# Kernel optimization log

Measured on AMD Instinct MI355X. Metric: run time of the kernel, lower is better.

The kernel has to match this reference:

```python
import jax, jax.numpy as jnp
import numpy as np

B, S, EMBED, DK, DV, M = 8, 1024, 1024, 512, 512, 64


def setup_inputs() -> dict:
    key = jax.random.key(0)
    ks = jax.random.split(key, 9)
    query_in = jax.random.normal(ks[0], (B, S, EMBED), dtype=jnp.float32)
    key_in = jax.random.normal(ks[1], (B, S, EMBED), dtype=jnp.float32)
    value_in = jax.random.normal(ks[2], (B, S, EMBED), dtype=jnp.float32)
    lim = 1.0 / np.sqrt(EMBED)  # nn.Linear default init range
    u = lambda k, shape: jax.random.uniform(k, shape, minval=-lim, maxval=lim, dtype=jnp.float32)
    return {
        'query_in': query_in, 'key_in': key_in, 'value_in': value_in,
        'Wq': u(ks[3], (DK, EMBED)), 'bq': u(ks[4], (DK,)),
        'Wk': u(ks[5], (DK, EMBED)), 'bk': u(ks[6], (DK,)),
        'Wv': u(ks[7], (DV, EMBED)), 'bv': u(ks[8], (DV,)),
    }


def _select_landmarks(k_proj, m):
    # Original code runs recursive RLS sampling (random, host-side) over the m
    # segment-rows of key.reshape(B, m, seg, d) and gathers m of them back,
    # then flattens to (B, S, d). We use a deterministic data-dependent
    # selection (rows ranked by squared norm) with identical gather structure.
    Bb, Ss, d = k_proj.shape
    seg = Ss // m
    kr = k_proj.reshape(Bb, m, seg, d)
    scores = jnp.sum(kr * kr, axis=(2, 3))                      # [B, m]
    idx = jnp.argsort(-scores, axis=1)                          # [B, m]
    land = jnp.take_along_axis(kr, idx[:, :, None, None], axis=1)
    return land.reshape(Bb, Ss, d)                              # [B, S, d]


def reference(query_in, key_in, value_in, Wq, bq, Wk, bk, Wv, bv):
    scaling = DK ** -0.25  # 1/sqrt(sqrt(d_k)), applied to both q and k
    q = (jnp.einsum('bse,de->bsd', query_in, Wq) + bq) * scaling
    k = (jnp.einsum('bse,de->bsd', key_in, Wk) + bk) * scaling
    v = jnp.einsum('bse,de->bsd', value_in, Wv) + bv

    kl = _select_landmarks(k, M)                                # [B, S, DK]
    # is_decoder_self_attn is hard-coded True upstream -> q_landmarks = q,
    # so kernel_2 == kernel_1.
    kernel_1 = jax.nn.softmax(jnp.einsum('bqd,bkd->bqk', q, kl), axis=-1)
    kernel_2 = kernel_1
    kernel_3 = jax.nn.softmax(jnp.einsum('bqd,bkd->bqk', q, k), axis=-1)

    k2_inv = jnp.linalg.pinv(kernel_2)                          # [B, S, S] batched SVD
    out = jnp.einsum('bqk,bkd->bqd', jnp.einsum('bqm,bmk->bqk', kernel_1, k2_inv),
                     jnp.einsum('bqk,bkd->bqd', kernel_3, v))
    # dropout is identity in eval mode
    return out
```

## Files before the change

### kernel.cpp

```cpp
#include <hip/hip_runtime.h>
#include <hip/hip_bf16.h>

#define SS   1024
#define DKK  512

typedef __hip_bfloat16 bf16;
typedef __attribute__((ext_vector_type(8))) short s16x8;
typedef __attribute__((ext_vector_type(8))) unsigned short u16x8;
typedef __attribute__((ext_vector_type(4))) float f32x4;

#define WS_W(z)  ((48ull << 20) + ((size_t)(z) << 20))
#define WS_ST    (51ull << 20)
#define WS_Q     (52ull << 20)
#define WS_K     (60ull << 20)
#define WS_VT    (68ull << 20)
#define WS_LG    (0ull)

__device__ __forceinline__ void async_ld16(const void* g, void* s) {
  __builtin_amdgcn_global_load_lds(
      (const __attribute__((address_space(1))) void*)g,
      (__attribute__((address_space(3))) void*)s, 16, 0, 0);
}

__device__ __forceinline__ unsigned short f2bfu(float f) {
  return __builtin_bit_cast(unsigned short, __float2bfloat16(f));
}
__device__ __forceinline__ float bfu2f(unsigned short u) {
  unsigned int i = ((unsigned int)u) << 16;
  return __builtin_bit_cast(float, i);
}

__global__ __launch_bounds__(256)
void convert_w(const float* __restrict__ w0, const float* __restrict__ w1,
               const float* __restrict__ w2, char* __restrict__ ws)
{
  const int bx = blockIdx.x;
  const int z = bx >> 8, local = bx & 255;
  const float* src = (z == 0) ? w0 : (z == 1) ? w1 : w2;
  unsigned short* dst = (unsigned short*)(ws + WS_W(z));
  const int i = local * 2048 + threadIdx.x * 8;
  const float4* s = (const float4*)(src + i);
  float4 a = s[0], b = s[1];
  ushort4 o0, o1;
  o0.x = f2bfu(a.x); o0.y = f2bfu(a.y); o0.z = f2bfu(a.z); o0.w = f2bfu(a.w);
  o1.x = f2bfu(b.x); o1.y = f2bfu(b.y); o1.z = f2bfu(b.z); o1.w = f2bfu(b.w);
  ((ushort4*)(dst + i))[0] = o0;
  ((ushort4*)(dst + i))[1] = o1;
}

template<int BM, int K, int LDA, int LDB>
__device__ __forceinline__ void gemm_core(const bf16* __restrict__ A,
                                          const bf16* __restrict__ Bw,
                                          int bm, int bn,
                                          short* As, short* Bs, f32x4* acc)
{
  constexpr int MI = BM / 32;
  constexpr int AR = BM / 4;
  const int tid  = threadIdx.x;
  const int lane = tid & 63;
  const int wave = tid >> 6;
  const int l8   = lane >> 3;
  const int kch  = ((lane & 7) ^ l8) * 8;
  const bf16* ag = A  + (size_t)(bm * BM + wave * AR + l8) * LDA + kch;
  const bf16* bg = Bw + (size_t)(bn * 128 + wave * 32 + l8) * LDB + kch;
  short* AsW = As + wave * AR * 64;
  short* BsW = Bs + wave * 32 * 64;
  const int waveM = wave >> 1, waveN = wave & 1;
  const int l16  = lane & 15;
  const int quad = lane >> 4;
  const int xr   = l16 & 7;

  #pragma unroll
  for (int t = 0; t < MI * 4; ++t)
    #pragma unroll
    for (int r = 0; r < 4; ++r) acc[t][r] = 0.0f;

  for (int kt = 0; kt < K / 64; ++kt) {
    #pragma unroll
    for (int j = 0; j < AR / 8; ++j) async_ld16(ag + (size_t)j * 8 * LDA, AsW + j * 8 * 64);
    #pragma unroll
    for (int j = 0; j < 4; ++j)      async_ld16(bg + (size_t)j * 8 * LDB, BsW + j * 8 * 64);
    ag += 64; bg += 64;
    __syncthreads();
    #pragma unroll
    for (int ks = 0; ks < 2; ++ks) {
      s16x8 af[MI], bfv[4];
      #pragma unroll
      for (int mi = 0; mi < MI; ++mi) {
        const int row  = waveM * (BM / 2) + mi * 16 + l16;
        const int slot = (ks * 4 + quad) ^ xr;
        af[mi] = *(const s16x8*)&As[row * 64 + slot * 8];
      }
      #pragma unroll
      for (int ni = 0; ni < 4; ++ni) {
        const int row  = waveN * 64 + ni * 16 + l16;
        const int slot = (ks * 4 + quad) ^ xr;
        bfv[ni] = *(const s16x8*)&Bs[row * 64 + slot * 8];
      }
      #pragma unroll
      for (int mi = 0; mi < MI; ++mi)
        #pragma unroll
        for (int ni = 0; ni < 4; ++ni)
          acc[mi * 4 + ni] = __builtin_amdgcn_mfma_f32_16x16x32_bf16(
              af[mi], bfv[ni], acc[mi * 4 + ni], 0, 0, 0);
    }
    __syncthreads();
  }
}

template<int K, int LDA, int LDB>
__device__ __forceinline__ void gemm_core_f32a(const float* __restrict__ A,
                                               const bf16* __restrict__ Bw,
                                               int bm, int bn,
                                               short* As, short* Bs, f32x4* acc)
{
  const int tid  = threadIdx.x;
  const int lane = tid & 63;
  const int wave = tid >> 6;
  const int l8   = lane >> 3;
  const int kch  = ((lane & 7) ^ l8) * 8;
  const bf16* bg = Bw + (size_t)(bn * 256 + wave * 64 + l8) * LDB + kch;
  short* BsW = Bs + wave * 64 * 64;
  const int arow = tid >> 3;
  const int ag8  = tid & 7;
  const int slotA = (ag8 ^ (arow & 7)) * 8;
  const float* ag = A + (size_t)(bm * 64 + arow) * LDA + ag8 * 8;
  const int waveM = wave >> 1, waveN = wave & 1;
  const int l16  = lane & 15;
  const int quad = lane >> 4;
  const int xr   = l16 & 7;

  #pragma unroll
  for (int t = 0; t < 16; ++t)
    #pragma unroll
    for (int r = 0; r < 4; ++r) acc[t][r] = 0.0f;

  for (int kt = 0; kt < K / 64; ++kt) {
    #pragma unroll
    for (int j = 0; j < 8; ++j) async_ld16(bg + (size_t)j * 8 * LDB, BsW + j * 8 * 64);
    bg += 64;
    #pragma unroll
    for (int p = 0; p < 2; ++p) {
      const float4* s = (const float4*)(ag + (size_t)p * 32 * LDA);
      float4 a = s[0], b = s[1];
      u16x8 v;
      v[0] = f2bfu(a.x); v[1] = f2bfu(a.y); v[2] = f2bfu(a.z); v[3] = f2bfu(a.w);
      v[4] = f2bfu(b.x); v[5] = f2bfu(b.y); v[6] = f2bfu(b.z); v[7] = f2bfu(b.w);
      *(u16x8*)&As[(p * 32 + arow) * 64 + slotA] = v;
    }
    ag += 64;
    __syncthreads();
    #pragma unroll
    for (int ks = 0; ks < 2; ++ks) {
      s16x8 af[2], bfv[8];
      #pragma unroll
      for (int mi = 0; mi < 2; ++mi) {
        const int row  = waveM * 32 + mi * 16 + l16;
        const int slot = (ks * 4 + quad) ^ xr;
        af[mi] = *(const s16x8*)&As[row * 64 + slot * 8];
      }
      #pragma unroll
      for (int ni = 0; ni < 8; ++ni) {
        const int row  = waveN * 128 + ni * 16 + l16;
        const int slot = (ks * 4 + quad) ^ xr;
        bfv[ni] = *(const s16x8*)&Bs[row * 64 + slot * 8];
      }
      #pragma unroll
      for (int mi = 0; mi < 2; ++mi)
        #pragma unroll
        for (int ni = 0; ni < 8; ++ni)
          acc[mi * 8 + ni] = __builtin_amdgcn_mfma_f32_16x16x32_bf16(
              af[mi], bfv[ni], acc[mi * 8 + ni], 0, 0, 0);
    }
    __syncthreads();
  }
}

__global__ __launch_bounds__(256, 3)
void proj_kernel(const float* __restrict__ Xq, const float* __restrict__ Xk,
                 const float* __restrict__ Xv, const bf16* __restrict__ W0,
                 const float* __restrict__ bq, const float* __restrict__ bk,
                 const float* __restrict__ bv,
                 bf16* __restrict__ qo, bf16* __restrict__ ko,
                 bf16* __restrict__ vT, float qscale)
{
  __shared__ __align__(16) short As[64 * 64];
  __shared__ __align__(16) short Bs[256 * 64];
  const int id   = blockIdx.x;
  const int xcd  = id & 7;
  const int s    = id >> 3;
  const int bn   = s & 1;
  const int pair = (s >> 1) * 8 + xcd;
  const int bm   = pair & 127;
  const int z    = pair >> 7;
  const float* A  = (z == 0) ? Xq : (z == 1) ? Xk : Xv;
  const bf16*  Bw = W0 + ((size_t)z << 19);
  const float* bias = (z == 0) ? bq : (z == 1) ? bk : bv;
  f32x4 acc[16];
  gemm_core_f32a<1024, 1024, 1024>(A, Bw, bm, bn, As, Bs, acc);

  const int lane = threadIdx.x & 63;
  const int wave = threadIdx.x >> 6;
  const int waveM = wave >> 1, waveN = wave & 1;
  const int l16 = lane & 15, quad = lane >> 4;
  const int row0 = bm * 64 + waveM * 32;
  const int col0 = bn * 256 + waveN * 128;
  const float sc = (z == 0) ? qscale : 1.0f;
  bf16* C = (z == 0) ? qo : ko;
  #pragma unroll
  for (int ni = 0; ni < 8; ++ni) {
    const int col = col0 + ni * 16 + l16;
    const float bb = bias[col];
    #pragma unroll
    for (int mi = 0; mi < 2; ++mi)
      #pragma unroll
      for (int r = 0; r < 4; ++r) {
        const int row = row0 + mi * 16 + quad * 4 + r;
        const float v = acc[mi * 8 + ni][r] + bb;
        if (z == 2)
          vT[((size_t)(row >> 10) * DKK + col) * SS + (row & (SS - 1))] =
              __float2bfloat16(v);
        else
          C[(size_t)row * DKK + col] = __float2bfloat16(v * sc);
      }
  }
}

__global__ __launch_bounds__(256, 4)
void scores_kernel(const bf16* __restrict__ q, const bf16* __restrict__ k,
                   bf16* __restrict__ lgB, float* __restrict__ stats)
{
  __shared__ __align__(16) short As[64 * 64];
  __shared__ __align__(16) short Bs[128 * 64];
  const int z = blockIdx.z;
  const int bn = blockIdx.x, bm = blockIdx.y;
  f32x4 acc[8];
  gemm_core<64, 512, 512, 512>(q + (size_t)z * SS * DKK, k + (size_t)z * SS * DKK,
                               bm, bn, As, Bs, acc);

  const int lane = threadIdx.x & 63;
  const int wave = threadIdx.x >> 6;
  const int waveM = wave >> 1, waveN = wave & 1;
  const int l16 = lane & 15, quad = lane >> 4;
  const int row0 = bm * 64 + waveM * 32;
  const int col0 = bn * 128 + waveN * 64;
  bf16* C = lgB + (size_t)z * SS * SS;
  #pragma unroll
  for (int ni = 0; ni < 4; ++ni) {
    const int col = col0 + ni * 16 + l16;
    #pragma unroll
    for (int mi = 0; mi < 2; ++mi)
      #pragma unroll
      for (int r = 0; r < 4; ++r) {
        const int row = row0 + mi * 16 + quad * 4 + r;
        C[(size_t)row * SS + col] = __float2bfloat16(acc[mi * 4 + ni][r]);
      }
  }
  const int chunk = bn * 2 + waveN;
  #pragma unroll
  for (int mi = 0; mi < 2; ++mi)
    #pragma unroll
    for (int r = 0; r < 4; ++r) {
      float xr4[4];
      float m = -1e30f;
      #pragma unroll
      for (int ni = 0; ni < 4; ++ni) {
        xr4[ni] = bfu2f(f2bfu(acc[mi * 4 + ni][r]));
        m = fmaxf(m, xr4[ni]);
      }
      #pragma unroll
      for (int msk = 1; msk < 16; msk <<= 1) m = fmaxf(m, __shfl_xor(m, msk));
      float e = 0.f;
      #pragma unroll
      for (int ni = 0; ni < 4; ++ni) e += __expf(xr4[ni] - m);
      #pragma unroll
      for (int msk = 1; msk < 16; msk <<= 1) e += __shfl_xor(e, msk);
      if (l16 == 0) {
        const int row = row0 + mi * 16 + quad * 4 + r;
        float2 mr; mr.x = m; mr.y = e;
        *(float2*)&stats[(((size_t)z * SS + row) * 16 + chunk) * 2] = mr;
      }
    }
}

__device__ __forceinline__ void gemm_core_pv(const unsigned short* __restrict__ lg,
                                             const bf16* __restrict__ vT,
                                             int bm, int bn,
                                             const float* Ml, const float* Rl,
                                             short* As, short* Bs, f32x4* acc)
{
  const int tid  = threadIdx.x;
  const int lane = tid & 63;
  const int wave = tid >> 6;
  const int l8   = lane >> 3;
  const int kch  = ((lane & 7) ^ l8) * 8;
  const bf16* bg = vT + (size_t)(bn * 128 + wave * 32 + l8) * 1024 + kch;
  short* BsW = Bs + wave * 32 * 64;
  const int arow = tid >> 3;
  const int ag8  = tid & 7;
  const int slotA = (ag8 ^ (arow & 7)) * 8;
  const unsigned short* ag = lg + (size_t)(bm * 64 + arow) * 1024 + ag8 * 8;
  const int waveM = wave >> 1, waveN = wave & 1;
  const int l16  = lane & 15;
  const int quad = lane >> 4;
  const int xr   = l16 & 7;

  #pragma unroll
  for (int t = 0; t < 8; ++t)
    #pragma unroll
    for (int r = 0; r < 4; ++r) acc[t][r] = 0.0f;

  for (int kt = 0; kt < 16; ++kt) {
    #pragma unroll
    for (int j = 0; j < 4; ++j) async_ld16(bg + (size_t)j * 8 * 1024, BsW + j * 8 * 64);
    bg += 64;
    #pragma unroll
    for (int p = 0; p < 2; ++p) {
      const int rl = p * 32 + arow;
      u16x8 u = *(const u16x8*)(ag + (size_t)p * 32 * 1024);
      const float M = Ml[rl], R = Rl[rl];
      u16x8 v;
      #pragma unroll
      for (int j = 0; j < 8; ++j)
        v[j] = f2bfu(__expf(bfu2f((unsigned short)u[j]) - M) * R);
      *(u16x8*)&As[rl * 64 + slotA] = v;
    }
    ag += 64;
    __syncthreads();
    #pragma unroll
    for (int ks = 0; ks < 2; ++ks) {
      s16x8 af[2], bfv[4];
      #pragma unroll
      for (int mi = 0; mi < 2; ++mi) {
        const int row  = waveM * 32 + mi * 16 + l16;
        const int slot = (ks * 4 + quad) ^ xr;
        af[mi] = *(const s16x8*)&As[row * 64 + slot * 8];
      }
      #pragma unroll
      for (int ni = 0; ni < 4; ++ni) {
        const int row  = waveN * 64 + ni * 16 + l16;
        const int slot = (ks * 4 + quad) ^ xr;
        bfv[ni] = *(const s16x8*)&Bs[row * 64 + slot * 8];
      }
      #pragma unroll
      for (int mi = 0; mi < 2; ++mi)
        #pragma unroll
        for (int ni = 0; ni < 4; ++ni)
          acc[mi * 4 + ni] = __builtin_amdgcn_mfma_f32_16x16x32_bf16(
              af[mi], bfv[ni], acc[mi * 4 + ni], 0, 0, 0);
    }
    __syncthreads();
  }
}

__global__ __launch_bounds__(256, 4)
void pv_kernel(const unsigned short* __restrict__ lgB, const bf16* __restrict__ vT,
               const float* __restrict__ stats, float* __restrict__ out)
{
  __shared__ __align__(16) short As[64 * 64];
  __shared__ __align__(16) short Bs[128 * 64];
  __shared__ float Ml[64], Rl[64];
  const int z = blockIdx.z;
  const int bn = blockIdx.x, bm = blockIdx.y;
  const int tid = threadIdx.x;

  if (tid < 64) {
    const int row = bm * 64 + tid;
    const float* st = stats + ((size_t)z * SS + row) * 32;
    float mc[16], lc[16];
    float M = -1e30f;
    #pragma unroll
    for (int c = 0; c < 16; ++c) {
      mc[c] = st[c * 2]; lc[c] = st[c * 2 + 1];
      M = fmaxf(M, mc[c]);
    }
    float L = 0.f;
    #pragma unroll
    for (int c = 0; c < 16; ++c) L += __expf(mc[c] - M) * lc[c];
    Ml[tid] = M; Rl[tid] = 1.0f / L;
  }
  __syncthreads();

  f32x4 acc[8];
  gemm_core_pv(lgB + (size_t)z * SS * SS, vT + (size_t)z * DKK * SS,
               bm, bn, Ml, Rl, As, Bs, acc);

  const int lane = tid & 63;
  const int wave = tid >> 6;
  const int waveM = wave >> 1, waveN = wave & 1;
  const int l16 = lane & 15, quad = lane >> 4;
  const int row0 = bm * 64 + waveM * 32;
  const int col0 = bn * 128 + waveN * 64;
  float* C = out + (size_t)z * SS * DKK;
  #pragma unroll
  for (int ni = 0; ni < 4; ++ni) {
    const int col = col0 + ni * 16 + l16;
    #pragma unroll
    for (int mi = 0; mi < 2; ++mi)
      #pragma unroll
      for (int r = 0; r < 4; ++r) {
        const int row = row0 + mi * 16 + quad * 4 + r;
        C[(size_t)row * DKK + col] = acc[mi * 4 + ni][r];
      }
  }
}

extern "C" void kernel_launch(void* const* d_in, const int* in_sizes, int n_in,
                              void* d_out, int out_size, void* d_ws, size_t ws_size,
                              hipStream_t stream)
{
  char* ws = (char*)d_ws;
  bf16*  W0   = (bf16*)(ws + WS_W(0));
  float* stat = (float*)(ws + WS_ST);
  bf16*  q    = (bf16*)(ws + WS_Q);
  bf16*  kk   = (bf16*)(ws + WS_K);
  bf16*  vT   = (bf16*)(ws + WS_VT);
  bf16*  lgB  = (bf16*)(ws + WS_LG);

  const float qscale = 0.044194173824159216f;

  dim3 blk(256, 1, 1);
  hipLaunchKernelGGL(convert_w, dim3(768), blk, 0, stream,
                     (const float*)d_in[3], (const float*)d_in[5],
                     (const float*)d_in[7], ws);
  hipLaunchKernelGGL(proj_kernel, dim3(768, 1, 1), blk, 0, stream,
                     (const float*)d_in[0], (const float*)d_in[1],
                     (const float*)d_in[2], W0,
                     (const float*)d_in[4], (const float*)d_in[6],
                     (const float*)d_in[8], q, kk, vT, qscale);
  hipLaunchKernelGGL(scores_kernel, dim3(8, 16, 8), blk, 0, stream,
                     q, kk, lgB, stat);
  hipLaunchKernelGGL(pv_kernel, dim3(4, 16, 8), blk, 0, stream,
                     (const unsigned short*)lgB, vT, stat, (float*)d_out);
}
```

Baseline: 219.9 us.

## Fuse score and PV kernels into a single online-softmax attention kernel

New measurement: 297.0 us. 1.35x slower.

```diff
diff --git a/kernel.cpp b/kernel.cpp
--- a/kernel.cpp
+++ b/kernel.cpp
@@ -10,11 +10,9 @@
 typedef __attribute__((ext_vector_type(4))) float f32x4;
 
 #define WS_W(z)  ((48ull << 20) + ((size_t)(z) << 20))
-#define WS_ST    (51ull << 20)
 #define WS_Q     (52ull << 20)
 #define WS_K     (60ull << 20)
 #define WS_VT    (68ull << 20)
-#define WS_LG    (0ull)
 
 __device__ __forceinline__ void async_ld16(const void* g, void* s) {
   __builtin_amdgcn_global_load_lds(
@@ -46,66 +44,6 @@
   o1.x = f2bfu(b.x); o1.y = f2bfu(b.y); o1.z = f2bfu(b.z); o1.w = f2bfu(b.w);
   ((ushort4*)(dst + i))[0] = o0;
   ((ushort4*)(dst + i))[1] = o1;
-}
-
-template<int BM, int K, int LDA, int LDB>
-__device__ __forceinline__ void gemm_core(const bf16* __restrict__ A,
-                                          const bf16* __restrict__ Bw,
-                                          int bm, int bn,
-                                          short* As, short* Bs, f32x4* acc)
-{
-  constexpr int MI = BM / 32;
-  constexpr int AR = BM / 4;
-  const int tid  = threadIdx.x;
-  const int lane = tid & 63;
-  const int wave = tid >> 6;
-  const int l8   = lane >> 3;
-  const int kch  = ((lane & 7) ^ l8) * 8;
-  const bf16* ag = A  + (size_t)(bm * BM + wave * AR + l8) * LDA + kch;
-  const bf16* bg = Bw + (size_t)(bn * 128 + wave * 32 + l8) * LDB + kch;
-  short* AsW = As + wave * AR * 64;
-  short* BsW = Bs + wave * 32 * 64;
-  const int waveM = wave >> 1, waveN = wave & 1;
-  const int l16  = lane & 15;
-  const int quad = lane >> 4;
-  const int xr   = l16 & 7;
-
-  #pragma unroll
-  for (int t = 0; t < MI * 4; ++t)
-    #pragma unroll
-    for (int r = 0; r < 4; ++r) acc[t][r] = 0.0f;
-
-  for (int kt = 0; kt < K / 64; ++kt) {
-    #pragma unroll
-    for (int j = 0; j < AR / 8; ++j) async_ld16(ag + (size_t)j * 8 * LDA, AsW + j * 8 * 64);
-    #pragma unroll
-    for (int j = 0; j < 4; ++j)      async_ld16(bg + (size_t)j * 8 * LDB, BsW + j * 8 * 64);
-    ag += 64; bg += 64;
-    __syncthreads();
-    #pragma unroll
-    for (int ks = 0; ks < 2; ++ks) {
-      s16x8 af[MI], bfv[4];
-      #pragma unroll
-      for (int mi = 0; mi < MI; ++mi) {
-        const int row  = waveM * (BM / 2) + mi * 16 + l16;
-        const int slot = (ks * 4 + quad) ^ xr;
-        af[mi] = *(const s16x8*)&As[row * 64 + slot * 8];
-      }
-      #pragma unroll
-      for (int ni = 0; ni < 4; ++ni) {
-        const int row  = waveN * 64 + ni * 16 + l16;
-        const int slot = (ks * 4 + quad) ^ xr;
-        bfv[ni] = *(const s16x8*)&Bs[row * 64 + slot * 8];
-      }
-      #pragma unroll
-      for (int mi = 0; mi < MI; ++mi)
-        #pragma unroll
-        for (int ni = 0; ni < 4; ++ni)
-          acc[mi * 4 + ni] = __builtin_amdgcn_mfma_f32_16x16x32_bf16(
-              af[mi], bfv[ni], acc[mi * 4 + ni], 0, 0, 0);
-    }
-    __syncthreads();
-  }
 }
 
 template<int K, int LDA, int LDB>
@@ -226,182 +164,190 @@
   }
 }
 
-__global__ __launch_bounds__(256, 4)
-void scores_kernel(const bf16* __restrict__ q, const bf16* __restrict__ k,
-                   bf16* __restrict__ lgB, float* __restrict__ stats)
-{
-  __shared__ __align__(16) short As[64 * 64];
-  __shared__ __align__(16) short Bs[128 * 64];
-  const int z = blockIdx.z;
-  const int bn = blockIdx.x, bm = blockIdx.y;
-  f32x4 acc[8];
-  gemm_core<64, 512, 512, 512>(q + (size_t)z * SS * DKK, k + (size_t)z * SS * DKK,
-                               bm, bn, As, Bs, acc);
-
-  const int lane = threadIdx.x & 63;
-  const int wave = threadIdx.x >> 6;
-  const int waveM = wave >> 1, waveN = wave & 1;
-  const int l16 = lane & 15, quad = lane >> 4;
-  const int row0 = bm * 64 + waveM * 32;
-  const int col0 = bn * 128 + waveN * 64;
-  bf16* C = lgB + (size_t)z * SS * SS;
-  #pragma unroll
-  for (int ni = 0; ni < 4; ++ni) {
-    const int col = col0 + ni * 16 + l16;
-    #pragma unroll
-    for (int mi = 0; mi < 2; ++mi)
-      #pragma unroll
-      for (int r = 0; r < 4; ++r) {
-        const int row = row0 + mi * 16 + quad * 4 + r;
-        C[(size_t)row * SS + col] = __float2bfloat16(acc[mi * 4 + ni][r]);
-      }
-  }
-  const int chunk = bn * 2 + waveN;
-  #pragma unroll
-  for (int mi = 0; mi < 2; ++mi)
-    #pragma unroll
-    for (int r = 0; r < 4; ++r) {
-      float xr4[4];
-      float m = -1e30f;
-      #pragma unroll
-      for (int ni = 0; ni < 4; ++ni) {
-        xr4[ni] = bfu2f(f2bfu(acc[mi * 4 + ni][r]));
-        m = fmaxf(m, xr4[ni]);
-      }
-      #pragma unroll
-      for (int msk = 1; msk < 16; msk <<= 1) m = fmaxf(m, __shfl_xor(m, msk));
-      float e = 0.f;
-      #pragma unroll
-      for (int ni = 0; ni < 4; ++ni) e += __expf(xr4[ni] - m);
-      #pragma unroll
-      for (int msk = 1; msk < 16; msk <<= 1) e += __shfl_xor(e, msk);
-      if (l16 == 0) {
-        const int row = row0 + mi * 16 + quad * 4 + r;
-        float2 mr; mr.x = m; mr.y = e;
-        *(float2*)&stats[(((size_t)z * SS + row) * 16 + chunk) * 2] = mr;
-      }
-    }
-}
-
-__device__ __forceinline__ void gemm_core_pv(const unsigned short* __restrict__ lg,
-                                             const bf16* __restrict__ vT,
-                                             int bm, int bn,
-                                             const float* Ml, const float* Rl,
-                                             short* As, short* Bs, f32x4* acc)
-{
+__global__ __launch_bounds__(256, 1)
+void attn_kernel(const bf16* __restrict__ q, const bf16* __restrict__ kk,
+                 const bf16* __restrict__ vT, float* __restrict__ out)
+{
+  __shared__ __align__(16) short Ps[32 * 64];
+  __shared__ __align__(16) float Mt[32 * 4];
+  __shared__ __align__(16) float Lt[32 * 4];
+
+  const int id = blockIdx.x;
+  const int z  = id & 7;
+  const int qb = id >> 3;
   const int tid  = threadIdx.x;
   const int lane = tid & 63;
-  const int wave = tid >> 6;
-  const int l8   = lane >> 3;
-  const int kch  = ((lane & 7) ^ l8) * 8;
-  const bf16* bg = vT + (size_t)(bn * 128 + wave * 32 + l8) * 1024 + kch;
-  short* BsW = Bs + wave * 32 * 64;
-  const int arow = tid >> 3;
-  const int ag8  = tid & 7;
-  const int slotA = (ag8 ^ (arow & 7)) * 8;
-  const unsigned short* ag = lg + (size_t)(bm * 64 + arow) * 1024 + ag8 * 8;
-  const int waveM = wave >> 1, waveN = wave & 1;
+  const int w    = tid >> 6;
   const int l16  = lane & 15;
   const int quad = lane >> 4;
-  const int xr   = l16 & 7;
-
-  #pragma unroll
-  for (int t = 0; t < 8; ++t)
+
+  const bf16* qz = q  + (size_t)z * SS * DKK;
+  const bf16* kz = kk + (size_t)z * SS * DKK;
+  const bf16* vz = vT + (size_t)z * DKK * SS;
+
+  s16x8 qf0[16], qf1[16];
+  {
+    const bf16* q0 = qz + (size_t)(qb * 32 + l16) * DKK + quad * 8;
+    const bf16* q1 = q0 + (size_t)16 * DKK;
+    #pragma unroll
+    for (int ks = 0; ks < 16; ++ks) {
+      qf0[ks] = *(const s16x8*)(q0 + ks * 32);
+      qf1[ks] = *(const s16x8*)(q1 + ks * 32);
+    }
+  }
+
+  const bf16* kfl = kz + (size_t)(w * 16 + l16) * DKK + quad * 8;
+  const bf16* vfl = vz + (size_t)(w * 128 + l16) * SS + quad * 8;
+
+  f32x4 acc[16];
+  #pragma unroll
+  for (int t = 0; t < 16; ++t)
     #pragma unroll
     for (int r = 0; r < 4; ++r) acc[t][r] = 0.0f;
 
-  for (int kt = 0; kt < 16; ++kt) {
-    #pragma unroll
-    for (int j = 0; j < 4; ++j) async_ld16(bg + (size_t)j * 8 * 1024, BsW + j * 8 * 64);
-    bg += 64;
-    #pragma unroll
-    for (int p = 0; p < 2; ++p) {
-      const int rl = p * 32 + arow;
-      u16x8 u = *(const u16x8*)(ag + (size_t)p * 32 * 1024);
-      const float M = Ml[rl], R = Rl[rl];
-      u16x8 v;
-      #pragma unroll
-      for (int j = 0; j < 8; ++j)
-        v[j] = f2bfu(__expf(bfu2f((unsigned short)u[j]) - M) * R);
-      *(u16x8*)&As[rl * 64 + slotA] = v;
-    }
-    ag += 64;
+  float mrun0[4], mrun1[4], lrun0[4], lrun1[4];
+  #pragma unroll
+  for (int r = 0; r < 4; ++r) {
+    mrun0[r] = -1e30f; mrun1[r] = -1e30f;
+    lrun0[r] = 0.0f;   lrun1[r] = 0.0f;
+  }
+
+  for (int it = 0; it < 16; ++it) {
+    const int kv0 = it * 64;
+    f32x4 s0, s1;
+    #pragma unroll
+    for (int r = 0; r < 4; ++r) { s0[r] = 0.0f; s1[r] = 0.0f; }
+    const bf16* kp = kfl + (size_t)kv0 * DKK;
+    #pragma unroll
+    for (int ks = 0; ks < 16; ++ks) {
+      const s16x8 bfk = *(const s16x8*)(kp + ks * 32);
+      s0 = __builtin_amdgcn_mfma_f32_16x16x32_bf16(qf0[ks], bfk, s0, 0, 0, 0);
+      s1 = __builtin_amdgcn_mfma_f32_16x16x32_bf16(qf1[ks], bfk, s1, 0, 0, 0);
+    }
+
+    float mt0[4], mt1[4];
+    #pragma unroll
+    for (int r = 0; r < 4; ++r) {
+      float v0 = s0[r], v1 = s1[r];
+      #pragma unroll
+      for (int msk = 1; msk < 16; msk <<= 1) {
+        v0 = fmaxf(v0, __shfl_xor(v0, msk));
+        v1 = fmaxf(v1, __shfl_xor(v1, msk));
+      }
+      mt0[r] = v0; mt1[r] = v1;
+    }
+    if (l16 == 0) {
+      #pragma unroll
+      for (int r = 0; r < 4; ++r) {
+        Mt[(quad * 4 + r) * 4 + w] = mt0[r];
+        Mt[(16 + quad * 4 + r) * 4 + w] = mt1[r];
+      }
+    }
     __syncthreads();
+
+    float al0[4], al1[4], p0[4], p1[4];
+    #pragma unroll
+    for (int r = 0; r < 4; ++r) {
+      {
+        const f32x4 mv = *(const f32x4*)&Mt[(quad * 4 + r) * 4];
+        const float mtile = fmaxf(fmaxf(mv[0], mv[1]), fmaxf(mv[2], mv[3]));
+        const float mnew = fmaxf(mrun0[r], mtile);
+        al0[r] = __expf(mrun0[r] - mnew);
+        mrun0[r] = mnew;
+        p0[r] = __expf(s0[r] - mnew);
+      }
+      {
+        const f32x4 mv = *(const f32x4*)&Mt[(16 + quad * 4 + r) * 4];
+        const float mtile = fmaxf(fmaxf(mv[0], mv[1]), fmaxf(mv[2], mv[3]));
+        const float mnew = fmaxf(mrun1[r], mtile);
+        al1[r] = __expf(mrun1[r] - mnew);
+        mrun1[r] = mnew;
+        p1[r] = __expf(s1[r] - mnew);
+      }
+    }
+    #pragma unroll
+    for (int r = 0; r < 4; ++r) {
+      float e0 = p0[r], e1 = p1[r];
+      #pragma unroll
+      for (int msk = 1; msk < 16; msk <<= 1) {
+        e0 += __shfl_xor(e0, msk);
+        e1 += __shfl_xor(e1, msk);
+      }
+      if (l16 == 0) {
+        Lt[(quad * 4 + r) * 4 + w] = e0;
+        Lt[(16 + quad * 4 + r) * 4 + w] = e1;
+      }
+    }
+    {
+      const int colP = w * 16 + l16;
+      const int c8 = colP >> 3, cb = colP & 7;
+      #pragma unroll
+      for (int r = 0; r < 4; ++r) {
+        {
+          const int row = quad * 4 + r;
+          Ps[row * 64 + ((c8 ^ ((row >> 1) & 7)) * 8) + cb] = (short)f2bfu(p0[r]);
+        }
+        {
+          const int row = 16 + quad * 4 + r;
+          Ps[row * 64 + ((c8 ^ ((row >> 1) & 7)) * 8) + cb] = (short)f2bfu(p1[r]);
+        }
+      }
+    }
+    __syncthreads();
+
+    #pragma unroll
+    for (int r = 0; r < 4; ++r) {
+      {
+        const f32x4 lv = *(const f32x4*)&Lt[(quad * 4 + r) * 4];
+        lrun0[r] = lrun0[r] * al0[r] + (lv[0] + lv[1] + lv[2] + lv[3]);
+      }
+      {
+        const f32x4 lv = *(const f32x4*)&Lt[(16 + quad * 4 + r) * 4];
+        lrun1[r] = lrun1[r] * al1[r] + (lv[0] + lv[1] + lv[2] + lv[3]);
+      }
+    }
+    #pragma unroll
+    for (int ni = 0; ni < 8; ++ni)
+      #pragma unroll
+      for (int r = 0; r < 4; ++r) {
+        acc[ni][r]     *= al0[r];
+        acc[8 + ni][r] *= al1[r];
+      }
+
+    const bf16* vp = vfl + kv0;
     #pragma unroll
     for (int ks = 0; ks < 2; ++ks) {
-      s16x8 af[2], bfv[4];
-      #pragma unroll
-      for (int mi = 0; mi < 2; ++mi) {
-        const int row  = waveM * 32 + mi * 16 + l16;
-        const int slot = (ks * 4 + quad) ^ xr;
-        af[mi] = *(const s16x8*)&As[row * 64 + slot * 8];
-      }
-      #pragma unroll
-      for (int ni = 0; ni < 4; ++ni) {
-        const int row  = waveN * 64 + ni * 16 + l16;
-        const int slot = (ks * 4 + quad) ^ xr;
-        bfv[ni] = *(const s16x8*)&Bs[row * 64 + slot * 8];
-      }
-      #pragma unroll
-      for (int mi = 0; mi < 2; ++mi)
-        #pragma unroll
-        for (int ni = 0; ni < 4; ++ni)
-          acc[mi * 4 + ni] = __builtin_amdgcn_mfma_f32_16x16x32_bf16(
-              af[mi], bfv[ni], acc[mi * 4 + ni], 0, 0, 0);
-    }
-    __syncthreads();
-  }
-}
-
-__global__ __launch_bounds__(256, 4)
-void pv_kernel(const unsigned short* __restrict__ lgB, const bf16* __restrict__ vT,
-               const float* __restrict__ stats, float* __restrict__ out)
-{
-  __shared__ __align__(16) short As[64 * 64];
-  __shared__ __align__(16) short Bs[128 * 64];
-  __shared__ float Ml[64], Rl[64];
-  const int z = blockIdx.z;
-  const int bn = blockIdx.x, bm = blockIdx.y;
-  const int tid = threadIdx.x;
-
-  if (tid < 64) {
-    const int row = bm * 64 + tid;
-    const float* st = stats + ((size_t)z * SS + row) * 32;
-    float mc[16], lc[16];
-    float M = -1e30f;
-    #pragma unroll
-    for (int c = 0; c < 16; ++c) {
-      mc[c] = st[c * 2]; lc[c] = st[c * 2 + 1];
-      M = fmaxf(M, mc[c]);
-    }
-    float L = 0.f;
-    #pragma unroll
-    for (int c = 0; c < 16; ++c) L += __expf(mc[c] - M) * lc[c];
-    Ml[tid] = M; Rl[tid] = 1.0f / L;
-  }
-  __syncthreads();
-
-  f32x4 acc[8];
-  gemm_core_pv(lgB + (size_t)z * SS * SS, vT + (size_t)z * DKK * SS,
-               bm, bn, Ml, Rl, As, Bs, acc);
-
-  const int lane = tid & 63;
-  const int wave = tid >> 6;
-  const int waveM = wave >> 1, waveN = wave & 1;
-  const int l16 = lane & 15, quad = lane >> 4;
-  const int row0 = bm * 64 + waveM * 32;
-  const int col0 = bn * 128 + waveN * 64;
-  float* C = out + (size_t)z * SS * DKK;
-  #pragma unroll
-  for (int ni = 0; ni < 4; ++ni) {
-    const int col = col0 + ni * 16 + l16;
-    #pragma unroll
-    for (int mi = 0; mi < 2; ++mi)
-      #pragma unroll
-      for (int r = 0; r < 4; ++r) {
-        const int row = row0 + mi * 16 + quad * 4 + r;
-        C[(size_t)row * DKK + col] = acc[mi * 4 + ni][r];
-      }
+      s16x8 pa0, pa1;
+      {
+        const int row = l16;
+        const int sl = (ks * 4 + quad) ^ ((row >> 1) & 7);
+        pa0 = *(const s16x8*)&Ps[row * 64 + sl * 8];
+      }
+      {
+        const int row = 16 + l16;
+        const int sl = (ks * 4 + quad) ^ ((row >> 1) & 7);
+        pa1 = *(const s16x8*)&Ps[row * 64 + sl * 8];
+      }
+      #pragma unroll
+      for (int ni = 0; ni < 8; ++ni) {
+        const s16x8 vf = *(const s16x8*)(vp + (size_t)ni * 16 * SS + ks * 32);
+        acc[ni]     = __builtin_amdgcn_mfma_f32_16x16x32_bf16(pa0, vf, acc[ni], 0, 0, 0);
+        acc[8 + ni] = __builtin_amdgcn_mfma_f32_16x16x32_bf16(pa1, vf, acc[8 + ni], 0, 0, 0);
+      }
+    }
+  }
+
+  float* oz = out + (size_t)z * SS * DKK;
+  #pragma unroll
+  for (int r = 0; r < 4; ++r) {
+    const float i0 = 1.0f / lrun0[r];
+    const float i1 = 1.0f / lrun1[r];
+    #pragma unroll
+    for (int ni = 0; ni < 8; ++ni) {
+      const int col = w * 128 + ni * 16 + l16;
+      oz[(size_t)(qb * 32 + quad * 4 + r) * DKK + col]      = acc[ni][r] * i0;
+      oz[(size_t)(qb * 32 + 16 + quad * 4 + r) * DKK + col] = acc[8 + ni][r] * i1;
+    }
   }
 }
 
@@ -411,11 +357,9 @@
 {
   char* ws = (char*)d_ws;
   bf16*  W0   = (bf16*)(ws + WS_W(0));
-  float* stat = (float*)(ws + WS_ST);
   bf16*  q    = (bf16*)(ws + WS_Q);
   bf16*  kk   = (bf16*)(ws + WS_K);
   bf16*  vT   = (bf16*)(ws + WS_VT);
-  bf16*  lgB  = (bf16*)(ws + WS_LG);
 
   const float qscale = 0.044194173824159216f;
 
@@ -428,8 +372,6 @@
                      (const float*)d_in[2], W0,
                      (const float*)d_in[4], (const float*)d_in[6],
                      (const float*)d_in[8], q, kk, vT, qscale);
-  hipLaunchKernelGGL(scores_kernel, dim3(8, 16, 8), blk, 0, stream,
-                     q, kk, lgB, stat);
-  hipLaunchKernelGGL(pv_kernel, dim3(4, 16, 8), blk, 0, stream,
-                     (const unsigned short*)lgB, vT, stat, (float*)d_out);
-}
+  hipLaunchKernelGGL(attn_kernel, dim3(256, 1, 1), blk, 0, stream,
+                     q, kk, vT, (float*)d_out);
+}
```

## Split softmax into standalone pass and use 128x128 tiles for score and PV GEMMs

Applied to the files above, without the earlier changes.

New measurement: 217.9 us. About the same (-0.9%).

```diff
diff --git a/kernel.cpp b/kernel.cpp
--- a/kernel.cpp
+++ b/kernel.cpp
@@ -10,7 +10,6 @@
 typedef __attribute__((ext_vector_type(4))) float f32x4;
 
 #define WS_W(z)  ((48ull << 20) + ((size_t)(z) << 20))
-#define WS_ST    (51ull << 20)
 #define WS_Q     (52ull << 20)
 #define WS_K     (60ull << 20)
 #define WS_VT    (68ull << 20)
@@ -226,177 +225,110 @@
   }
 }
 
-__global__ __launch_bounds__(256, 4)
+__global__ __launch_bounds__(256, 2)
 void scores_kernel(const bf16* __restrict__ q, const bf16* __restrict__ k,
-                   bf16* __restrict__ lgB, float* __restrict__ stats)
-{
-  __shared__ __align__(16) short As[64 * 64];
+                   bf16* __restrict__ lgB)
+{
+  __shared__ __align__(16) short As[128 * 64];
   __shared__ __align__(16) short Bs[128 * 64];
-  const int z = blockIdx.z;
-  const int bn = blockIdx.x, bm = blockIdx.y;
-  f32x4 acc[8];
-  gemm_core<64, 512, 512, 512>(q + (size_t)z * SS * DKK, k + (size_t)z * SS * DKK,
-                               bm, bn, As, Bs, acc);
+  const int id = blockIdx.x;
+  const int z  = id & 7;
+  const int s  = id >> 3;
+  const int bm = s & 7;
+  const int bn = s >> 3;
+  f32x4 acc[16];
+  gemm_core<128, 512, 512, 512>(q + (size_t)z * SS * DKK, k + (size_t)z * SS * DKK,
+                                bm, bn, As, Bs, acc);
 
   const int lane = threadIdx.x & 63;
   const int wave = threadIdx.x >> 6;
   const int waveM = wave >> 1, waveN = wave & 1;
   const int l16 = lane & 15, quad = lane >> 4;
-  const int row0 = bm * 64 + waveM * 32;
+  const int row0 = bm * 128 + waveM * 64;
   const int col0 = bn * 128 + waveN * 64;
   bf16* C = lgB + (size_t)z * SS * SS;
   #pragma unroll
   for (int ni = 0; ni < 4; ++ni) {
     const int col = col0 + ni * 16 + l16;
     #pragma unroll
-    for (int mi = 0; mi < 2; ++mi)
+    for (int mi = 0; mi < 4; ++mi)
       #pragma unroll
       for (int r = 0; r < 4; ++r) {
         const int row = row0 + mi * 16 + quad * 4 + r;
         C[(size_t)row * SS + col] = __float2bfloat16(acc[mi * 4 + ni][r]);
       }
   }
-  const int chunk = bn * 2 + waveN;
-  #pragma unroll
-  for (int mi = 0; mi < 2; ++mi)
-    #pragma unroll
-    for (int r = 0; r < 4; ++r) {
-      float xr4[4];
-      float m = -1e30f;
-      #pragma unroll
-      for (int ni = 0; ni < 4; ++ni) {
-        xr4[ni] = bfu2f(f2bfu(acc[mi * 4 + ni][r]));
-        m = fmaxf(m, xr4[ni]);
-      }
-      #pragma unroll
-      for (int msk = 1; msk < 16; msk <<= 1) m = fmaxf(m, __shfl_xor(m, msk));
-      float e = 0.f;
-      #pragma unroll
-      for (int ni = 0; ni < 4; ++ni) e += __expf(xr4[ni] - m);
-      #pragma unroll
-      for (int msk = 1; msk < 16; msk <<= 1) e += __shfl_xor(e, msk);
-      if (l16 == 0) {
-        const int row = row0 + mi * 16 + quad * 4 + r;
-        float2 mr; mr.x = m; mr.y = e;
-        *(float2*)&stats[(((size_t)z * SS + row) * 16 + chunk) * 2] = mr;
-      }
-    }
-}
-
-__device__ __forceinline__ void gemm_core_pv(const unsigned short* __restrict__ lg,
-                                             const bf16* __restrict__ vT,
-                                             int bm, int bn,
-                                             const float* Ml, const float* Rl,
-                                             short* As, short* Bs, f32x4* acc)
-{
-  const int tid  = threadIdx.x;
-  const int lane = tid & 63;
-  const int wave = tid >> 6;
-  const int l8   = lane >> 3;
-  const int kch  = ((lane & 7) ^ l8) * 8;
-  const bf16* bg = vT + (size_t)(bn * 128 + wave * 32 + l8) * 1024 + kch;
-  short* BsW = Bs + wave * 32 * 64;
-  const int arow = tid >> 3;
-  const int ag8  = tid & 7;
-  const int slotA = (ag8 ^ (arow & 7)) * 8;
-  const unsigned short* ag = lg + (size_t)(bm * 64 + arow) * 1024 + ag8 * 8;
-  const int waveM = wave >> 1, waveN = wave & 1;
-  const int l16  = lane & 15;
-  const int quad = lane >> 4;
-  const int xr   = l16 & 7;
-
-  #pragma unroll
-  for (int t = 0; t < 8; ++t)
-    #pragma unroll
-    for (int r = 0; r < 4; ++r) acc[t][r] = 0.0f;
-
-  for (int kt = 0; kt < 16; ++kt) {
-    #pragma unroll
-    for (int j = 0; j < 4; ++j) async_ld16(bg + (size_t)j * 8 * 1024, BsW + j * 8 * 64);
-    bg += 64;
-    #pragma unroll
-    for (int p = 0; p < 2; ++p) {
-      const int rl = p * 32 + arow;
-      u16x8 u = *(const u16x8*)(ag + (size_t)p * 32 * 1024);
-      const float M = Ml[rl], R = Rl[rl];
-      u16x8 v;
-      #pragma unroll
-      for (int j = 0; j < 8; ++j)
-        v[j] = f2bfu(__expf(bfu2f((unsigned short)u[j]) - M) * R);
-      *(u16x8*)&As[rl * 64 + slotA] = v;
-    }
-    ag += 64;
-    __syncthreads();
-    #pragma unroll
-    for (int ks = 0; ks < 2; ++ks) {
-      s16x8 af[2], bfv[4];
-      #pragma unroll
-      for (int mi = 0; mi < 2; ++mi) {
-        const int row  = waveM * 32 + mi * 16 + l16;
-        const int slot = (ks * 4 + quad) ^ xr;
-        af[mi] = *(const s16x8*)&As[row * 64 + slot * 8];
-      }
-      #pragma unroll
-      for (int ni = 0; ni < 4; ++ni) {
-        const int row  = waveN * 64 + ni * 16 + l16;
-        const int slot = (ks * 4 + quad) ^ xr;
-        bfv[ni] = *(const s16x8*)&Bs[row * 64 + slot * 8];
-      }
-      #pragma unroll
-      for (int mi = 0; mi < 2; ++mi)
-        #pragma unroll
-        for (int ni = 0; ni < 4; ++ni)
-          acc[mi * 4 + ni] = __builtin_amdgcn_mfma_f32_16x16x32_bf16(
-              af[mi], bfv[ni], acc[mi * 4 + ni], 0, 0, 0);
-    }
-    __syncthreads();
-  }
-}
-
-__global__ __launch_bounds__(256, 4)
-void pv_kernel(const unsigned short* __restrict__ lgB, const bf16* __restrict__ vT,
-               const float* __restrict__ stats, float* __restrict__ out)
-{
-  __shared__ __align__(16) short As[64 * 64];
+}
+
+__global__ __launch_bounds__(256)
+void softmax_p(unsigned short* __restrict__ lg)
+{
+  const int id = blockIdx.x;
+  const int z  = id & 7;
+  const int rb = id >> 3;
+  const int w    = threadIdx.x >> 6;
+  const int lane = threadIdx.x & 63;
+  const int row  = rb * 4 + w;
+  unsigned short* p = lg + ((size_t)z * SS + row) * SS + lane * 16;
+
+  u16x8 a = *(const u16x8*)p;
+  u16x8 b = *(const u16x8*)(p + 8);
+  float xf[16];
+  #pragma unroll
+  for (int j = 0; j < 8; ++j) { xf[j] = bfu2f(a[j]); xf[8 + j] = bfu2f(b[j]); }
+
+  float m = xf[0];
+  #pragma unroll
+  for (int j = 1; j < 16; ++j) m = fmaxf(m, xf[j]);
+  #pragma unroll
+  for (int msk = 1; msk < 64; msk <<= 1) m = fmaxf(m, __shfl_xor(m, msk));
+
+  float e[16];
+  float L = 0.f;
+  #pragma unroll
+  for (int j = 0; j < 16; ++j) { e[j] = __expf(xf[j] - m); L += e[j]; }
+  #pragma unroll
+  for (int msk = 1; msk < 64; msk <<= 1) L += __shfl_xor(L, msk);
+  const float R = 1.0f / L;
+
+  u16x8 o0, o1;
+  #pragma unroll
+  for (int j = 0; j < 8; ++j) {
+    o0[j] = f2bfu(e[j] * R);
+    o1[j] = f2bfu(e[8 + j] * R);
+  }
+  *(u16x8*)p = o0;
+  *(u16x8*)(p + 8) = o1;
+}
+
+__global__ __launch_bounds__(256, 2)
+void pv_kernel(const bf16* __restrict__ P, const bf16* __restrict__ vT,
+               float* __restrict__ out)
+{
+  __shared__ __align__(16) short As[128 * 64];
   __shared__ __align__(16) short Bs[128 * 64];
-  __shared__ float Ml[64], Rl[64];
-  const int z = blockIdx.z;
-  const int bn = blockIdx.x, bm = blockIdx.y;
-  const int tid = threadIdx.x;
-
-  if (tid < 64) {
-    const int row = bm * 64 + tid;
-    const float* st = stats + ((size_t)z * SS + row) * 32;
-    float mc[16], lc[16];
-    float M = -1e30f;
-    #pragma unroll
-    for (int c = 0; c < 16; ++c) {
-      mc[c] = st[c * 2]; lc[c] = st[c * 2 + 1];
-      M = fmaxf(M, mc[c]);
-    }
-    float L = 0.f;
-    #pragma unroll
-    for (int c = 0; c < 16; ++c) L += __expf(mc[c] - M) * lc[c];
-    Ml[tid] = M; Rl[tid] = 1.0f / L;
-  }
-  __syncthreads();
-
-  f32x4 acc[8];
-  gemm_core_pv(lgB + (size_t)z * SS * SS, vT + (size_t)z * DKK * SS,
-               bm, bn, Ml, Rl, As, Bs, acc);
-
-  const int lane = tid & 63;
-  const int wave = tid >> 6;
+  const int id = blockIdx.x;
+  const int z  = id & 7;
+  const int s  = id >> 3;
+  const int bm = s & 7;
+  const int bn = s >> 3;
+  f32x4 acc[16];
+  gemm_core<128, 1024, 1024, 1024>(P + (size_t)z * SS * SS,
+                                   vT + (size_t)z * DKK * SS,
+                                   bm, bn, As, Bs, acc);
+
+  const int lane = threadIdx.x & 63;
+  const int wave = threadIdx.x >> 6;
   const int waveM = wave >> 1, waveN = wave & 1;
   const int l16 = lane & 15, quad = lane >> 4;
-  const int row0 = bm * 64 + waveM * 32;
+  const int row0 = bm * 128 + waveM * 64;
   const int col0 = bn * 128 + waveN * 64;
   float* C = out + (size_t)z * SS * DKK;
   #pragma unroll
   for (int ni = 0; ni < 4; ++ni) {
     const int col = col0 + ni * 16 + l16;
     #pragma unroll
-    for (int mi = 0; mi < 2; ++mi)
+    for (int mi = 0; mi < 4; ++mi)
       #pragma unroll
       for (int r = 0; r < 4; ++r) {
         const int row = row0 + mi * 16 + quad * 4 + r;
@@ -411,7 +343,6 @@
 {
   char* ws = (char*)d_ws;
   bf16*  W0   = (bf16*)(ws + WS_W(0));
-  float* stat = (float*)(ws + WS_ST);
   bf16*  q    = (bf16*)(ws + WS_Q);
   bf16*  kk   = (bf16*)(ws + WS_K);
   bf16*  vT   = (bf16*)(ws + WS_VT);
@@ -428,8 +359,10 @@
                      (const float*)d_in[2], W0,
                      (const float*)d_in[4], (const float*)d_in[6],
                      (const float*)d_in[8], q, kk, vT, qscale);
-  hipLaunchKernelGGL(scores_kernel, dim3(8, 16, 8), blk, 0, stream,
-                     q, kk, lgB, stat);
-  hipLaunchKernelGGL(pv_kernel, dim3(4, 16, 8), blk, 0, stream,
-                     (const unsigned short*)lgB, vT, stat, (float*)d_out);
-}
+  hipLaunchKernelGGL(scores_kernel, dim3(512, 1, 1), blk, 0, stream,
+                     q, kk, lgB);
+  hipLaunchKernelGGL(softmax_p, dim3(2048, 1, 1), blk, 0, stream,
+                     (unsigned short*)lgB);
+  hipLaunchKernelGGL(pv_kernel, dim3(256, 1, 1), blk, 0, stream,
+                     lgB, vT, (float*)d_out);
+}
```
